# Optimization experiments

Hardware: AMD Instinct MI355X
Metric: run time of the kernel (lower is better)

The kernel has to match this reference:

```python
import jax, jax.numpy as jnp
import numpy as np

V = 778   # MANO mesh vertex count (hard-coded in the module)
K = 9     # spiral neighborhood length
C = 256   # in_channels
OUT = 3   # out_channels (per-vertex offset xyz)
B3 = 192  # 3 * B, B = 64


def setup_inputs() -> dict:
    key = jax.random.key(0)
    ks = jax.random.split(key, 12)
    x = jax.random.normal(ks[0], (B3, V, C), jnp.float32)
    pred_occ = jax.random.normal(ks[1], (B3, 2, 5), jnp.float32)
    indices = jax.random.randint(ks[2], (V, K), 0, V)
    finger_sizes = [112, 120, 124, 116, 108]
    fingers = {f"finger{i}": jax.random.randint(ks[3 + i], (n,), 0, V)
               for i, n in enumerate(finger_sizes)}

    def lin(k, fan_in, fan_out):
        kw, kb = jax.random.split(k)
        w = jax.random.normal(kw, (fan_in, fan_out), jnp.float32) / np.float32(np.sqrt(fan_in))
        b = jax.random.normal(kb, (fan_out,), jnp.float32) * 0.01
        return w, b

    w0, b0 = lin(ks[8], 2 * C * K, 2 * C)
    w1, b1 = lin(ks[9], 2 * C * K, C)
    w2, b2 = lin(ks[10], C * K, C)
    wh, bh = lin(ks[11], C * K, OUT)
    return {"x": x, "pred_occ": pred_occ, "indices": indices, **fingers,
            "w0": w0, "b0": b0, "w1": w1, "b1": b1, "w2": w2, "b2": b2,
            "wh": wh, "bh": bh}


def spiral_conv(x, idx, w, b):
    # x: [B, V, Cin], idx: [V, K] -> gather spiral neighbors, flatten, linear
    B = x.shape[0]
    g = x[:, idx.reshape(-1), :].reshape(B, V, -1)  # [B, V, K*Cin]
    return g @ w + b


def reference(x, pred_occ, indices, finger0, finger1, finger2, finger3, finger4,
              w0, b0, w1, b1, w2, b2, wh, bh):
    # Per-finger non-occlusion probabilities: softmax over class dim, take class 0
    occ = jax.nn.softmax(pred_occ, axis=1)[:, 0, :5]          # [3B, 5]
    weights = jnp.ones((x.shape[0], V), x.dtype)
    for i, fidx in enumerate([finger0, finger1, finger2, finger3, finger4]):
        val = jnp.broadcast_to(occ[:, i:i + 1], (x.shape[0], fidx.shape[0]))
        weights = weights.at[:, fidx].set(val)
    B = x.shape[0] // 3
    wv = jnp.stack(jnp.split(weights, 3, axis=0), axis=-1)[..., None]  # [B, V, 3, 1]
    wv = jax.nn.softmax(wv, axis=2)
    xv = jnp.stack(jnp.split(x, 3, axis=0), axis=2)                    # [B, V, 3, C]
    wx = jnp.sum(wv * xv, axis=2)                                      # [B, V, C]
    h = jnp.concatenate([wx, x[:B]], axis=2)                           # [B, V, 2C]
    h = jax.nn.relu(spiral_conv(h, indices, w0, b0))
    h = jax.nn.relu(spiral_conv(h, indices, w1, b1))
    h = jax.nn.relu(spiral_conv(h, indices, w2, b2))
    return spiral_conv(h, indices, wh, bh)                             # [B, V, 3]
```

## Files before the change

### kernel.cpp

```cpp
#include <hip/hip_runtime.h>

typedef unsigned short ushort_t;
typedef __attribute__((ext_vector_type(8))) __bf16 bf16x8;
typedef __attribute__((ext_vector_type(8))) unsigned short ushort8;
typedef __attribute__((ext_vector_type(4))) float floatx4;
typedef __attribute__((ext_vector_type(16))) float floatx16;

#define VN 778
#define KNB 9

__device__ __forceinline__ float bf2f(unsigned short s) {
  union { unsigned int u; float f; } x; x.u = ((unsigned int)s) << 16; return x.f;
}
__device__ __forceinline__ unsigned short f2bf(float f) {
  union { float f; unsigned int u; } x; x.f = f;
  unsigned int r = x.u + 0x7fffu + ((x.u >> 16) & 1u);
  return (unsigned short)(r >> 16);
}

__device__ __forceinline__ void load_lds16(const void* g, void* l) {
  __builtin_amdgcn_global_load_lds(
      (const __attribute__((address_space(1))) unsigned int*)g,
      (__attribute__((address_space(3))) unsigned int*)l, 16, 0, 0);
}

__device__ __forceinline__ int xcd_swizzle(int g, int nwg) {
  int q = nwg >> 3, r = nwg & 7;
  int xcd = g & 7, o = g >> 3;
  return (xcd < r ? xcd * (q + 1) : r * (q + 1) + (xcd - r) * q) + o;
}

__global__ void prep_misc(const float* __restrict__ pred_occ,
                          const int* f0, const int* f1, const int* f2,
                          const int* f3, const int* f4,
                          int n0, int n1, int n2, int n3, int n4,
                          const float* __restrict__ wh,
                          float* __restrict__ occ, int* __restrict__ fid,
                          float* __restrict__ whT) {
  int t = threadIdx.x;
  for (int i = t; i < 192 * 5; i += 256) {
    int r = i / 5, f = i % 5;
    float p0 = pred_occ[r * 10 + f];
    float p1 = pred_occ[r * 10 + 5 + f];
    occ[i] = 1.0f / (1.0f + __expf(p1 - p0));
  }
  for (int i = t; i < VN; i += 256) fid[i] = -1;
  __syncthreads();
  const int* fp[5] = {f0, f1, f2, f3, f4};
  int fn[5] = {n0, n1, n2, n3, n4};
  for (int fi = 0; fi < 5; ++fi) {
    for (int i = t; i < fn[fi]; i += 256) fid[fp[fi][i]] = fi;
    __syncthreads();
  }
  for (int i = t; i < 3 * 2304; i += 256) {
    int o = i / 2304, k = i % 2304;
    whT[i] = wh[k * 3 + o];
  }
}

__global__ void wx_kernel(const float* __restrict__ x, const float* __restrict__ occ,
                          const int* __restrict__ fid, ushort_t* __restrict__ wx,
                          ushort_t* __restrict__ xb) {
  int g = blockIdx.x * 256 + threadIdx.x;
  int c8 = (g & 31) << 3;
  int bv = g >> 5;
  int b = bv / VN;
  int v = bv - b * VN;
  int f = fid[v];
  float w0 = 1.f, w1 = 1.f, w2 = 1.f;
  if (f >= 0) {
    w0 = occ[b * 5 + f];
    w1 = occ[(64 + b) * 5 + f];
    w2 = occ[(128 + b) * 5 + f];
  }
  float m = fmaxf(w0, fmaxf(w1, w2));
  float e0 = __expf(w0 - m), e1 = __expf(w1 - m), e2 = __expf(w2 - m);
  float inv = 1.0f / (e0 + e1 + e2);
  e0 *= inv; e1 *= inv; e2 *= inv;
  size_t base = (size_t)bv * 256 + c8;
  size_t obase = ((size_t)(v * 64 + b)) * 256 + c8;
  const size_t V1 = (size_t)64 * VN * 256, V2 = (size_t)128 * VN * 256;
  floatx4 x0a = *(const floatx4*)(x + base);
  floatx4 x0b = *(const floatx4*)(x + base + 4);
  floatx4 x1a = *(const floatx4*)(x + V1 + base);
  floatx4 x1b = *(const floatx4*)(x + V1 + base + 4);
  floatx4 x2a = *(const floatx4*)(x + V2 + base);
  floatx4 x2b = *(const floatx4*)(x + V2 + base + 4);
  ushort8 o, xo;
#pragma unroll
  for (int e = 0; e < 4; ++e) {
    o[e]     = f2bf(e0 * x0a[e] + e1 * x1a[e] + e2 * x2a[e]);
    o[e + 4] = f2bf(e0 * x0b[e] + e1 * x1b[e] + e2 * x2b[e]);
    xo[e]     = f2bf(x0a[e]);
    xo[e + 4] = f2bf(x0b[e]);
  }
  *(ushort8*)(wx + obase) = o;
  if (xb) *(ushort8*)(xb + obase) = xo;
}

__global__ void pack_all(const float* __restrict__ w0, const float* __restrict__ w1,
                         const float* __restrict__ w2, ushort_t* __restrict__ wP0,
                         ushort_t* __restrict__ wP1, ushort_t* __restrict__ wP2) {
  int chunk = blockIdx.x * 256 + threadIdx.x;
  const float* w; ushort_t* wP; int N, ksn;
  if (chunk < 294912)       { w = w0; wP = wP0; N = 512; ksn = 288; }
  else if (chunk < 442368)  { chunk -= 294912; w = w1; wP = wP1; N = 256; ksn = 288; }
  else                      { chunk -= 442368; w = w2; wP = wP2; N = 256; ksn = 144; }
  int lane = chunk & 63;
  int rest = chunk >> 6;
  int ks = rest % ksn;
  int tn = rest / ksn;
  int n = (tn << 5) + (lane & 31);
  int kb = (ks << 4) + ((lane >> 5) << 3);
  ushort8 o;
#pragma unroll
  for (int j = 0; j < 8; ++j) o[j] = f2bf(w[(size_t)(kb + j) * N + n]);
  *(ushort8*)(wP + (size_t)chunk * 8) = o;
}

template <int CIN, int MODE>
__global__ __launch_bounds__(512, 4) void spiral_gemm(
    const ushort_t* __restrict__ act0, const float* __restrict__ actF,
    const ushort_t* __restrict__ actB, const ushort_t* __restrict__ wP,
    const float* __restrict__ bias, const int* __restrict__ idx,
    ushort_t* __restrict__ out, int NOUT, int nbx) {
  constexpr int H = CIN / 128;
  constexpr int P = KNB * H;
  __shared__ __align__(16) ushort_t Alds[2][2048 * 8];
  const int wgid = xcd_swizzle(blockIdx.x, gridDim.x);
  const int yb = wgid / nbx;
  const int xb = wgid - yb * nbx;
  const int v0 = xb * 2;
  const int n0 = yb << 8;
  const int tid = threadIdx.x;
  const int lane = tid & 63;
  const int wv = tid >> 6;
  const int mlo = lane & 31;
  const int q = lane >> 5;
  const int xm = mlo & 7;
  floatx16 acc0{}, acc1{}, acc2{}, acc3{};
  const int KtotSteps = KNB * (CIN / 16);
  const int tn0 = (n0 >> 5) + wv;
  const ushort_t* bp = wP + (size_t)tn0 * KtotSteps * 512 + lane * 8;
  const int* iv0 = idx + v0 * KNB;
  const int* iv1 = iv0 + KNB;
  const int aoff0 = mlo * 128;
  const int aoff1 = (mlo + 32) * 128;
  const int aoff2 = 8192 + mlo * 128;
  const int aoff3 = 8192 + (mlo + 32) * 128;

  auto dma_stage = [&](int p, ushort_t* buf) {
    const int nbr = p / H, h = p - nbr * H;
    const int nva = iv0[nbr], nvb = iv1[nbr];
#pragma unroll
    for (int it = 0; it < 4; ++it) {
      const int slotb = ((wv << 2) + it) << 6;
      const int s = slotb + lane;
      const int vv = s >> 10;
      const int row = (s >> 4) & 63;
      const int ck = (s & 15) ^ (row & 7);
      const int nv = vv ? nvb : nva;
      const ushort_t* src;
      if (MODE == 0) {
        src = act0 + ((size_t)(nv * 64 + row)) * CIN + h * 128 + ck * 8;
      } else {
        const ushort_t* basep = (MODE == 1 || h < 2) ? act0 : actB;
        src = basep + ((size_t)(nv * 64 + row)) * 256 + (h & 1) * 128 + ck * 8;
      }
      load_lds16(src, buf + (size_t)slotb * 8);
    }
  };
  auto f32_stage = [&](int p, ushort_t* buf) {
    const int nbr = p / H, h = p - nbr * H;
    const int nva = iv0[nbr], nvb = iv1[nbr];
#pragma unroll
    for (int j = 0; j < 4; ++j) {
      const int s = (j << 9) + tid;
      const int vv = s >> 10;
      const int row = (s >> 4) & 63;
      const int ck = (s & 15) ^ (row & 7);
      const int nv = vv ? nvb : nva;
      const float* src = actF + ((size_t)(row * VN + nv)) * 256 + (h - 2) * 128 + ck * 8;
      floatx4 fa = *(const floatx4*)src;
      floatx4 fb = *(const floatx4*)(src + 4);
      ushort8 o;
#pragma unroll
      for (int e = 0; e < 4; ++e) { o[e] = f2bf(fa[e]); o[e + 4] = f2bf(fb[e]); }
      *(ushort8*)(buf + (size_t)s * 8) = o;
    }
  };

  dma_stage(0, Alds[0]);
  __syncthreads();
#pragma unroll 2
  for (int p = 0; p < P; ++p) {
    ushort_t* cur = Alds[p & 1];
    ushort_t* nxt = Alds[(p + 1) & 1];
    const bool have_next = (p + 1 < P);
    const bool next_f32 = (MODE == 1) && (((p + 1) & (H - 1)) >= 2);
    if (have_next && !next_f32) dma_stage(p + 1, nxt);
#pragma unroll
    for (int ks = 0; ks < 8; ++ks) {
      const int cko = ((((ks << 1) + q) ^ xm) << 3);
      bf16x8 a0 = *(const bf16x8*)(cur + aoff0 + cko);
      bf16x8 a1 = *(const bf16x8*)(cur + aoff1 + cko);
      bf16x8 a2 = *(const bf16x8*)(cur + aoff2 + cko);
      bf16x8 a3 = *(const bf16x8*)(cur + aoff3 + cko);
      bf16x8 bv = *(const bf16x8*)bp; bp += 512;
      acc0 = __builtin_amdgcn_mfma_f32_32x32x16_bf16(a0, bv, acc0, 0, 0, 0);
      acc1 = __builtin_amdgcn_mfma_f32_32x32x16_bf16(a1, bv, acc1, 0, 0, 0);
      acc2 = __builtin_amdgcn_mfma_f32_32x32x16_bf16(a2, bv, acc2, 0, 0, 0);
      acc3 = __builtin_amdgcn_mfma_f32_32x32x16_bf16(a3, bv, acc3, 0, 0, 0);
    }
    __syncthreads();
    if (have_next && next_f32) { f32_stage(p + 1, nxt); __syncthreads(); }
  }
  const int n = n0 + (wv << 5) + mlo;
  const float bn = bias[n];
#pragma unroll
  for (int t = 0; t < 4; ++t) {
    const floatx16 av = (t == 0) ? acc0 : (t == 1) ? acc1 : (t == 2) ? acc2 : acc3;
    const int vcur = v0 + (t >> 1);
    const int bbase = (t & 1) << 5;
#pragma unroll
    for (int r = 0; r < 16; ++r) {
      const int m = (r & 3) + ((r >> 2) << 3) + (q << 2);
      float val = av[r] + bn; val = val > 0.f ? val : 0.f;
      out[((size_t)(vcur * 64 + bbase + m)) * NOUT + n] = f2bf(val);
    }
  }
}

__global__ void head_kernel(const ushort_t* __restrict__ act, const float* __restrict__ whT,
                            const float* __restrict__ bh, const int* __restrict__ idx,
                            float* __restrict__ out) {
  __shared__ __align__(16) ushort_t Alds[64 * 256];
  __shared__ float red[3][4][64];
  const int v = xcd_swizzle(blockIdx.x, gridDim.x);
  const int tid = threadIdx.x;
  const int b = tid & 63;
  const int kc = tid >> 6;
  const int xm = b & 7;
  float a0 = 0.f, a1 = 0.f, a2 = 0.f;
  for (int nbr = 0; nbr < KNB; ++nbr) {
    const int nv = idx[v * KNB + nbr];
    __syncthreads();
#pragma unroll
    for (int it = 0; it < 8; ++it) {
      int L = it * 256 + tid;
      int bb = L >> 5;
      int jj = L & 31;
      ushort8 val = *(const ushort8*)(act + ((size_t)(nv * 64 + bb)) * 256 + (jj << 3));
      int slot = jj ^ (bb & 7);
      *(ushort8*)&Alds[(size_t)(bb * 32 + slot) * 8] = val;
    }
    __syncthreads();
    const float* wp = whT + nbr * 256;
#pragma unroll
    for (int j0 = 0; j0 < 8; ++j0) {
      int j = (kc << 3) + j0;
      int jj = j ^ xm;
      ushort8 a8 = *(const ushort8*)&Alds[(b * 32 + jj) * 8];
#pragma unroll
      for (int e = 0; e < 8; ++e) {
        float av = bf2f(a8[e]);
        int k = (j << 3) + e;
        a0 += av * wp[k];
        a1 += av * wp[2304 + k];
        a2 += av * wp[4608 + k];
      }
    }
  }
  red[0][kc][b] = a0;
  red[1][kc][b] = a1;
  red[2][kc][b] = a2;
  __syncthreads();
  if (tid < 64) {
    float s0 = red[0][0][b] + red[0][1][b] + red[0][2][b] + red[0][3][b];
    float s1 = red[1][0][b] + red[1][1][b] + red[1][2][b] + red[1][3][b];
    float s2 = red[2][0][b] + red[2][1][b] + red[2][2][b] + red[2][3][b];
    size_t o = ((size_t)(b * VN + v)) * 3;
    out[o + 0] = s0 + bh[0];
    out[o + 1] = s1 + bh[1];
    out[o + 2] = s2 + bh[2];
  }
}

extern "C" void kernel_launch(void* const* d_in, const int* in_sizes, int n_in,
                              void* d_out, int out_size, void* d_ws, size_t ws_size,
                              hipStream_t stream) {
  const float* x        = (const float*)d_in[0];
  const float* pred_occ = (const float*)d_in[1];
  const int* indices    = (const int*)d_in[2];
  const int* f0 = (const int*)d_in[3];
  const int* f1 = (const int*)d_in[4];
  const int* f2 = (const int*)d_in[5];
  const int* f3 = (const int*)d_in[6];
  const int* f4 = (const int*)d_in[7];
  const float* w0 = (const float*)d_in[8];
  const float* b0 = (const float*)d_in[9];
  const float* w1 = (const float*)d_in[10];
  const float* b1 = (const float*)d_in[11];
  const float* w2 = (const float*)d_in[12];
  const float* b2 = (const float*)d_in[13];
  const float* wh = (const float*)d_in[14];
  const float* bh = (const float*)d_in[15];
  float* outp = (float*)d_out;

  char* ws = (char*)d_ws;
  ushort_t* wP0 = (ushort_t*)(ws + 0);
  ushort_t* wP1 = (ushort_t*)(ws + 4718592);
  ushort_t* wP2 = (ushort_t*)(ws + 7077888);
  float* whT    = (float*)(ws + 8257536);
  float* occ    = (float*)(ws + 8285184);
  int* fid      = (int*)(ws + 8289024);
  ushort_t* R0  = (ushort_t*)(ws + 8292352);
  ushort_t* R1  = (ushort_t*)(ws + 33785856);
  ushort_t* XB  = (ushort_t*)(ws + 84772864);
  const bool useXB = (ws_size >= 110266368ull);

  prep_misc<<<1, 256, 0, stream>>>(pred_occ, f0, f1, f2, f3, f4,
                                   in_sizes[3], in_sizes[4], in_sizes[5],
                                   in_sizes[6], in_sizes[7], wh, occ, fid, whT);
  pack_all<<<516096 / 256, 256, 0, stream>>>(w0, w1, w2, wP0, wP1, wP2);
  wx_kernel<<<6224, 256, 0, stream>>>(x, occ, fid, R0, useXB ? XB : nullptr);

  if (useXB)
    spiral_gemm<512, 2><<<778, 512, 0, stream>>>(R0, nullptr, XB, wP0, b0,
                                                 indices, R1, 512, 389);
  else
    spiral_gemm<512, 1><<<778, 512, 0, stream>>>(R0, x, nullptr, wP0, b0,
                                                 indices, R1, 512, 389);
  spiral_gemm<512, 0><<<389, 512, 0, stream>>>(R1, nullptr, nullptr, wP1, b1,
                                               indices, R0, 256, 389);
  spiral_gemm<256, 0><<<389, 512, 0, stream>>>(R0, nullptr, nullptr, wP2, b2,
                                               indices, R1, 256, 389);
  head_kernel<<<VN, 256, 0, stream>>>(R1, whT, bh, indices, outp);
  (void)n_in; (void)out_size;
}
```

Baseline: 806.9 us.

## Restructure spiral head as scatter by source vertex plus reduction pass

The head layer becomes a two-pass scatter. Each block loads one vertex's activation tile once, scans the spiral index table for every place that vertex appears, and writes per-slot partial dot products to a workspace buffer; a second kernel sums the nine slot contributions and adds the bias. This removes the nine gathered 32KB activation loads per block. In exchange it adds a full index scan per block, extra syncs per use, a workspace round trip, and a 256-use cap that would leave slots unwritten if one vertex were referenced more often.

```diff
diff --git a/kernel.cpp b/kernel.cpp
--- a/kernel.cpp
+++ b/kernel.cpp
@@ -231,59 +231,85 @@
   }
 }
 
-__global__ void head_kernel(const ushort_t* __restrict__ act, const float* __restrict__ whT,
-                            const float* __restrict__ bh, const int* __restrict__ idx,
-                            float* __restrict__ out) {
+__global__ void head_pass1(const ushort_t* __restrict__ act, const float* __restrict__ whT,
+                           const int* __restrict__ idx, float* __restrict__ contrib) {
   __shared__ __align__(16) ushort_t Alds[64 * 256];
   __shared__ float red[3][4][64];
-  const int v = xcd_swizzle(blockIdx.x, gridDim.x);
+  __shared__ int list[256];
+  __shared__ int lcnt;
+  const int v = blockIdx.x;
   const int tid = threadIdx.x;
+  if (tid == 0) lcnt = 0;
+#pragma unroll
+  for (int it = 0; it < 8; ++it) {
+    int L = it * 256 + tid;
+    int bb = L >> 5;
+    int jj = L & 31;
+    ushort8 val = *(const ushort8*)(act + ((size_t)(v * 64 + bb)) * 256 + (jj << 3));
+    int slot = jj ^ (bb & 7);
+    *(ushort8*)&Alds[(size_t)(bb * 32 + slot) * 8] = val;
+  }
+  __syncthreads();
+  for (int j = tid; j < VN * KNB; j += 256) {
+    if (idx[j] == v) {
+      int pos = atomicAdd(&lcnt, 1);
+      if (pos < 256) list[pos] = j;
+    }
+  }
+  __syncthreads();
+  const int nd = lcnt < 256 ? lcnt : 256;
   const int b = tid & 63;
   const int kc = tid >> 6;
   const int xm = b & 7;
-  float a0 = 0.f, a1 = 0.f, a2 = 0.f;
-  for (int nbr = 0; nbr < KNB; ++nbr) {
-    const int nv = idx[v * KNB + nbr];
-    __syncthreads();
-#pragma unroll
-    for (int it = 0; it < 8; ++it) {
-      int L = it * 256 + tid;
-      int bb = L >> 5;
-      int jj = L & 31;
-      ushort8 val = *(const ushort8*)(act + ((size_t)(nv * 64 + bb)) * 256 + (jj << 3));
-      int slot = jj ^ (bb & 7);
-      *(ushort8*)&Alds[(size_t)(bb * 32 + slot) * 8] = val;
-    }
-    __syncthreads();
-    const float* wp = whT + nbr * 256;
+  for (int i = 0; i < nd; ++i) {
+    const int j = list[i];
+    const int k = j % KNB;
+    const float* wp = whT + k * 256;
+    float a0 = 0.f, a1 = 0.f, a2 = 0.f;
 #pragma unroll
     for (int j0 = 0; j0 < 8; ++j0) {
-      int j = (kc << 3) + j0;
-      int jj = j ^ xm;
-      ushort8 a8 = *(const ushort8*)&Alds[(b * 32 + jj) * 8];
+      int jcol = (kc << 3) + j0;
+      int jj2 = jcol ^ xm;
+      ushort8 a8 = *(const ushort8*)&Alds[(b * 32 + jj2) * 8];
 #pragma unroll
       for (int e = 0; e < 8; ++e) {
         float av = bf2f(a8[e]);
-        int k = (j << 3) + e;
-        a0 += av * wp[k];
-        a1 += av * wp[2304 + k];
-        a2 += av * wp[4608 + k];
+        int c = (jcol << 3) + e;
+        a0 += av * wp[c];
+        a1 += av * wp[2304 + c];
+        a2 += av * wp[4608 + c];
       }
     }
-  }
-  red[0][kc][b] = a0;
-  red[1][kc][b] = a1;
-  red[2][kc][b] = a2;
-  __syncthreads();
-  if (tid < 64) {
-    float s0 = red[0][0][b] + red[0][1][b] + red[0][2][b] + red[0][3][b];
-    float s1 = red[1][0][b] + red[1][1][b] + red[1][2][b] + red[1][3][b];
-    float s2 = red[2][0][b] + red[2][1][b] + red[2][2][b] + red[2][3][b];
-    size_t o = ((size_t)(b * VN + v)) * 3;
-    out[o + 0] = s0 + bh[0];
-    out[o + 1] = s1 + bh[1];
-    out[o + 2] = s2 + bh[2];
-  }
+    red[0][kc][b] = a0;
+    red[1][kc][b] = a1;
+    red[2][kc][b] = a2;
+    __syncthreads();
+    if (tid < 64) {
+      float s0 = red[0][0][b] + red[0][1][b] + red[0][2][b] + red[0][3][b];
+      float s1 = red[1][0][b] + red[1][1][b] + red[1][2][b] + red[1][3][b];
+      float s2 = red[2][0][b] + red[2][1][b] + red[2][2][b] + red[2][3][b];
+      float* cp = contrib + (size_t)j * 192 + b * 3;
+      cp[0] = s0; cp[1] = s1; cp[2] = s2;
+    }
+    __syncthreads();
+  }
+}
+
+__global__ void head_pass2(const float* __restrict__ contrib, const float* __restrict__ bh,
+                           float* __restrict__ out) {
+  int g = blockIdx.x * 256 + threadIdx.x;
+  if (g >= 64 * VN) return;
+  int b = g / VN;
+  int u = g - b * VN;
+  float s0 = bh[0], s1 = bh[1], s2 = bh[2];
+  const float* cp = contrib + (size_t)u * KNB * 192 + b * 3;
+#pragma unroll
+  for (int k = 0; k < KNB; ++k) {
+    s0 += cp[0]; s1 += cp[1]; s2 += cp[2];
+    cp += 192;
+  }
+  size_t o = (size_t)g * 3;
+  out[o + 0] = s0; out[o + 1] = s1; out[o + 2] = s2;
 }
 
 extern "C" void kernel_launch(void* const* d_in, const int* in_sizes, int n_in,
@@ -317,6 +343,7 @@
   ushort_t* R0  = (ushort_t*)(ws + 8292352);
   ushort_t* R1  = (ushort_t*)(ws + 33785856);
   ushort_t* XB  = (ushort_t*)(ws + 84772864);
+  float* contrib = (float*)(ws + 0);
   const bool useXB = (ws_size >= 110266368ull);
 
   prep_misc<<<1, 256, 0, stream>>>(pred_occ, f0, f1, f2, f3, f4,
@@ -335,6 +362,7 @@
                                                indices, R0, 256, 389);
   spiral_gemm<256, 0><<<389, 512, 0, stream>>>(R0, nullptr, nullptr, wP2, b2,
                                                indices, R1, 256, 389);
-  head_kernel<<<VN, 256, 0, stream>>>(R1, whT, bh, indices, outp);
+  head_pass1<<<VN, 256, 0, stream>>>(R1, whT, indices, contrib);
+  head_pass2<<<195, 256, 0, stream>>>(contrib, bh, outp);
   (void)n_in; (void)out_size;
 }
```

After: 835.3 us. +3.5%, slower.
